# Performance work log

Measured on AMD Instinct MI355X. Metric: run time of the kernel, lower is better.

The kernel has to match this reference:

```python
import jax, jax.numpy as jnp
import numpy as np

B, S, D, H, F, L, V = 8, 512, 768, 12, 3072, 12, 30522
DK = D // H
SCALE = 1.0 / float(np.sqrt(DK))


def _ln(x, g, b, eps):
    mu = jnp.mean(x, -1, keepdims=True)
    var = jnp.mean((x - mu) ** 2, -1, keepdims=True)
    return (x - mu) / jnp.sqrt(var + eps) * g + b


def setup_inputs() -> dict:
    key = jax.random.key(0)
    ks = jax.random.split(key, 16)
    s = 0.02
    d = {
        'input_ids': jax.random.randint(ks[0], (B, S), 0, V),
        'token_type_ids': jax.random.randint(ks[1], (B, S), 0, 2),
        'attention_mask': jnp.ones((B, S), jnp.float32),
        'word_emb': jax.random.normal(ks[2], (V, D), jnp.float32) * s,
        'pos_emb': jax.random.normal(ks[3], (512, D), jnp.float32) * s,
        'type_emb': jax.random.normal(ks[4], (2, D), jnp.float32) * s,
        'emb_ln_g': jnp.ones((D,), jnp.float32),
        'emb_ln_b': jnp.zeros((D,), jnp.float32),
        # per-layer stacked params (torch Linear convention: W is [out,in])
        'Wq': jax.random.normal(ks[5], (L, D, D), jnp.float32) * s,
        'bq': jnp.zeros((L, D), jnp.float32),
        'Wk': jax.random.normal(ks[6], (L, D, D), jnp.float32) * s,
        'bk': jnp.zeros((L, D), jnp.float32),
        'Wv': jax.random.normal(ks[7], (L, D, D), jnp.float32) * s,
        'bv': jnp.zeros((L, D), jnp.float32),
        'Wo': jax.random.normal(ks[8], (L, D, D), jnp.float32) * s,
        'bo': jnp.zeros((L, D), jnp.float32),
        'attn_ln_g': jnp.ones((L, D), jnp.float32),
        'attn_ln_b': jnp.zeros((L, D), jnp.float32),
        'W1': jax.random.normal(ks[9], (L, F, D), jnp.float32) * s,
        'b1': jnp.zeros((L, F), jnp.float32),
        'W2': jax.random.normal(ks[10], (L, D, F), jnp.float32) * s,
        'b2': jnp.zeros((L, D), jnp.float32),
        'ffn_ln_g': jnp.ones((L, D), jnp.float32),
        'ffn_ln_b': jnp.zeros((L, D), jnp.float32),
    }
    return d


def reference(input_ids, token_type_ids, attention_mask, word_emb, pos_emb,
              type_emb, emb_ln_g, emb_ln_b, Wq, bq, Wk, bk, Wv, bv, Wo, bo,
              attn_ln_g, attn_ln_b, W1, b1, W2, b2, ffn_ln_g, ffn_ln_b):
    # Embeddings (dropout = identity in eval)
    x = word_emb[input_ids] + type_emb[token_type_ids] + pos_emb[:S][None]
    x = _ln(x, emb_ln_g, emb_ln_b, 1e-12)

    mask0 = attention_mask[:, None, None, :] == 0  # (B,1,1,S)

    def step(x, p):
        wq, bq_, wk, bk_, wv, bv_, wo, bo_, ag, ab, w1, b1_, w2, b2_, fg, fb = p
        q = (jnp.einsum('bsd,ed->bse', x, wq) + bq_).reshape(B, S, H, DK).transpose(0, 2, 1, 3)
        k = (jnp.einsum('bsd,ed->bse', x, wk) + bk_).reshape(B, S, H, DK).transpose(0, 2, 1, 3)
        v = (jnp.einsum('bsd,ed->bse', x, wv) + bv_).reshape(B, S, H, DK).transpose(0, 2, 1, 3)
        attn = jnp.einsum('bhqd,bhkd->bhqk', q, k) * SCALE  # (B,H,S,S)
        attn = jnp.where(mask0, -1e9, attn)
        p_attn = jax.nn.softmax(attn, axis=-1)
        ctx = jnp.einsum('bhqk,bhkd->bhqd', p_attn, v).transpose(0, 2, 1, 3).reshape(B, S, D)
        a = _ln(jnp.einsum('bsd,ed->bse', ctx, wo) + bo_ + x, ag, ab, 1e-5)
        # FFN: NO activation, and final LN has NO residual (faithful to source)
        h = jnp.einsum('bsd,fd->bsf', a, w1) + b1_
        y = jnp.einsum('bsf,df->bsd', h, w2) + b2_
        return _ln(y, fg, fb, 1e-5), None

    x, _ = jax.lax.scan(step, x, (Wq, bq, Wk, bk, Wv, bv, Wo, bo,
                                  attn_ln_g, attn_ln_b, W1, b1, W2, b2,
                                  ffn_ln_g, ffn_ln_b))
    return x
```

## Files before the change

kernel.cpp:

```cpp
#include <hip/hip_runtime.h>
#include <hip/hip_bf16.h>
#include <cstdint>
#include <cstddef>

typedef __bf16 bf16;
typedef __bf16 bf16x8 __attribute__((ext_vector_type(8)));
typedef __bf16 bf16x4 __attribute__((ext_vector_type(4)));
typedef float  floatx4 __attribute__((ext_vector_type(4)));

__device__ __forceinline__ void gload_lds16(const bf16* g, bf16* l) {
    __builtin_amdgcn_global_load_lds((const __attribute__((address_space(1))) void*)g,
                                     (__attribute__((address_space(3))) void*)l, 16, 0, 0);
}

__device__ __forceinline__ floatx4 mfma16(bf16x8 a, bf16x8 b, floatx4 c) {
    return __builtin_amdgcn_mfma_f32_16x16x32_bf16(a, b, c, 0, 0, 0);
}

template<int MODE, int TN>
__global__ __launch_bounds__(256)
void gemm_bt(const bf16* __restrict__ A, const bf16* __restrict__ Bw,
             const float* __restrict__ bias0, const float* __restrict__ bias1,
             const float* __restrict__ bias2,
             float* __restrict__ Cf, bf16* __restrict__ Cb0,
             bf16* __restrict__ Cb1, bf16* __restrict__ Cb2,
             int M, int N, int K)
{
    constexpr int NJ = TN / 32;
    __shared__ __attribute__((aligned(16))) bf16 As[128 * 32];
    __shared__ __attribute__((aligned(16))) bf16 Bs[TN * 32];

    const int tid  = threadIdx.x;
    const int lane = tid & 63;
    const int wv   = tid >> 6;
    const int quad = lane >> 4;
    const int l16  = lane & 15;
    const int m0   = blockIdx.y * 128;
    const int n0   = blockIdx.x * TN;
    const int wm   = wv & 1;
    const int wn   = wv >> 1;

    floatx4 acc[4][NJ] = {};

    const int srow = lane >> 2;
    const int scol = (lane & 3) * 8;
    const bf16* gA0 = A  + (size_t)(m0 + wv * 16 + srow) * K + scol;
    const bf16* gA1 = gA0 + (size_t)64 * K;
    const bf16* gB0 = Bw + (size_t)(n0 + wv * 16 + srow) * K + scol;
    const bf16* gB1 = gB0 + (size_t)64 * K;
    bf16* lA0 = &As[wv * 512];
    bf16* lA1 = &As[2048 + wv * 512];
    bf16* lB0 = &Bs[wv * 512];
    bf16* lB1 = &Bs[2048 + wv * 512];

    for (int k0 = 0; k0 < K; k0 += 32) {
        gload_lds16(gA0 + k0, lA0);
        gload_lds16(gA1 + k0, lA1);
        gload_lds16(gB0 + k0, lB0);
        if (TN == 128) gload_lds16(gB1 + k0, lB1);
        __syncthreads();

        bf16x8 af[4], bfr[NJ];
        #pragma unroll
        for (int i = 0; i < 4; ++i)
            af[i] = *(const bf16x8*)&As[(wm * 64 + i * 16 + l16) * 32 + quad * 8];
        #pragma unroll
        for (int j = 0; j < NJ; ++j)
            bfr[j] = *(const bf16x8*)&Bs[(wn * NJ * 16 + j * 16 + l16) * 32 + quad * 8];

        #pragma unroll
        for (int i = 0; i < 4; ++i)
            #pragma unroll
            for (int j = 0; j < NJ; ++j)
                acc[i][j] = mfma16(af[i], bfr[j], acc[i][j]);
        __syncthreads();
    }

    #pragma unroll
    for (int i = 0; i < 4; ++i) {
        const int rbase = m0 + wm * 64 + i * 16 + quad * 4;
        #pragma unroll
        for (int j = 0; j < NJ; ++j) {
            const int col = n0 + wn * NJ * 16 + j * 16 + l16;
            if (MODE == 0) {
                const float bv = bias0[col];
                #pragma unroll
                for (int r = 0; r < 4; ++r)
                    Cf[(size_t)(rbase + r) * N + col] = acc[i][j][r] + bv;
            } else if (MODE == 1) {
                const float bv = bias0[col];
                #pragma unroll
                for (int r = 0; r < 4; ++r)
                    Cb0[(size_t)(rbase + r) * N + col] = (bf16)(acc[i][j][r] + bv);
            } else {
                const int sel = col / 768;
                const int cc  = col - sel * 768;
                if (sel < 2) {
                    bf16* dst = (sel == 0) ? Cb0 : Cb1;
                    const float bv = ((sel == 0) ? bias0 : bias1)[cc];
                    #pragma unroll
                    for (int r = 0; r < 4; ++r)
                        dst[(size_t)(rbase + r) * 768 + cc] = (bf16)(acc[i][j][r] + bv);
                } else {
                    const float bv = bias2[cc];
                    const int bb = rbase >> 9, s = rbase & 511;
                    const int h = cc >> 6, d = cc & 63;
                    bf16x4 o;
                    #pragma unroll
                    for (int r = 0; r < 4; ++r) o[r] = (bf16)(acc[i][j][r] + bv);
                    *(bf16x4*)(Cb2 + (((size_t)(bb * 12 + h) * 64 + d) * 512 + s)) = o;
                }
            }
        }
    }
}

__global__ __launch_bounds__(256)
void cvt_all(const float* __restrict__ Wq, const float* __restrict__ Wk,
             const float* __restrict__ Wv, const float* __restrict__ Wo,
             const float* __restrict__ W1, const float* __restrict__ W2,
             bf16* __restrict__ out)
{
    const int l = blockIdx.y;
    const size_t i = ((size_t)blockIdx.x * 256 + threadIdx.x) * 8;
    const size_t wdd = 589824, wdf = 2359296;
    const float* src;
    size_t off;
    if      (i <  589824) { src = Wq + l * wdd; off = i; }
    else if (i < 1179648) { src = Wk + l * wdd; off = i - 589824; }
    else if (i < 1769472) { src = Wv + l * wdd; off = i - 1179648; }
    else if (i < 2359296) { src = Wo + l * wdd; off = i - 1769472; }
    else if (i < 4718592) { src = W1 + l * wdf; off = i - 2359296; }
    else                  { src = W2 + l * wdf; off = i - 4718592; }
    const float4 v0 = *(const float4*)(src + off);
    const float4 v1 = *(const float4*)(src + off + 4);
    bf16x8 o;
    o[0] = (bf16)v0.x; o[1] = (bf16)v0.y; o[2] = (bf16)v0.z; o[3] = (bf16)v0.w;
    o[4] = (bf16)v1.x; o[5] = (bf16)v1.y; o[6] = (bf16)v1.z; o[7] = (bf16)v1.w;
    *(bf16x8*)(out + (size_t)l * 7077888 + i) = o;
}

__global__ __launch_bounds__(256)
void attn3(const bf16* __restrict__ Q, const bf16* __restrict__ Kb,
           const bf16* __restrict__ VT, const float* __restrict__ mask,
           bf16* __restrict__ CTX)
{
    __shared__ __attribute__((aligned(16))) bf16 Ks[2][64 * 64];
    __shared__ __attribute__((aligned(16))) bf16 Vs[2][64 * 64];
    __shared__ __attribute__((aligned(16))) bf16 Ps[4 * 16 * 72];
    __shared__ float mb[512];

    const int tid  = threadIdx.x;
    const int lane = tid & 63;
    const int w    = tid >> 6;
    const int quad = lane >> 4;
    const int l16  = lane & 15;
    const int qt = blockIdx.x, h = blockIdx.y, b = blockIdx.z;

    mb[tid]       = (mask[b * 512 + tid] == 0.f)       ? -1e9f : -16.0f;
    mb[tid + 256] = (mask[b * 512 + tid + 256] == 0.f) ? -1e9f : -16.0f;

    bf16x8 qf0, qf1;
    {
        const bf16* qp = Q + (size_t)(b * 512 + qt * 64 + w * 16 + l16) * 768 + h * 64;
        qf0 = *(const bf16x8*)(qp + quad * 8);
        qf1 = *(const bf16x8*)(qp + 32 + quad * 8);
    }

    float lsum[4] = {0.f, 0.f, 0.f, 0.f};
    floatx4 accO[4] = {};
    bf16* pw = &Ps[w * 1152];

    const int srow8 = lane >> 3;
    const int scol8 = ((lane & 7) * 8) ^ (srow8 << 3);
    const int r0b   = w * 16;

    auto stageKV = [&](int kt, int bi) {
        #pragma unroll
        for (int i = 0; i < 2; ++i) {
            const int r0 = r0b + i * 8;
            gload_lds16(Kb + (size_t)(b * 512 + kt * 64 + r0 + srow8) * 768 + h * 64 + scol8,
                        &Ks[bi][r0 * 64]);
            gload_lds16(VT + ((size_t)(b * 12 + h) * 64 + r0 + srow8) * 512 + kt * 64 + scol8,
                        &Vs[bi][r0 * 64]);
        }
    };

    stageKV(0, 0);
    int cur = 0;
    const int swm = (l16 & 7) << 3;

    for (int kt = 0; kt < 8; ++kt) {
        __syncthreads();
        if (kt < 7) stageKV(kt + 1, cur ^ 1);

        #pragma unroll
        for (int ct = 0; ct < 4; ++ct) {
            const bf16x8 kf0 = *(const bf16x8*)&Ks[cur][(ct * 16 + l16) * 64 + ((quad * 8) ^ swm)];
            const bf16x8 kf1 = *(const bf16x8*)&Ks[cur][(ct * 16 + l16) * 64 + ((quad * 8 + 32) ^ swm)];
            floatx4 a = {0.f, 0.f, 0.f, 0.f};
            a = mfma16(qf0, kf0, a);
            a = mfma16(qf1, kf1, a);
            const float mbv = mb[kt * 64 + ct * 16 + l16];
            #pragma unroll
            for (int r = 0; r < 4; ++r) {
                const float p = __expf(fmaf(a[r], 0.125f, mbv));
                lsum[r] += p;
                pw[(quad * 4 + r) * 72 + ct * 16 + l16] = (bf16)p;
            }
        }

        #pragma unroll
        for (int kc = 0; kc < 2; ++kc) {
            const bf16x8 af = *(const bf16x8*)&pw[l16 * 72 + kc * 32 + quad * 8];
            #pragma unroll
            for (int ct2 = 0; ct2 < 4; ++ct2) {
                const bf16x8 bv = *(const bf16x8*)&Vs[cur][(ct2 * 16 + l16) * 64 + ((kc * 32 + quad * 8) ^ swm)];
                accO[ct2] = mfma16(af, bv, accO[ct2]);
            }
        }
        cur ^= 1;
    }

    float inv[4];
    #pragma unroll
    for (int r = 0; r < 4; ++r) {
        float s = lsum[r];
        #pragma unroll
        for (int o = 1; o < 16; o <<= 1) s += __shfl_xor(s, o);
        inv[r] = 1.0f / s;
    }
    #pragma unroll
    for (int ct2 = 0; ct2 < 4; ++ct2)
        #pragma unroll
        for (int r = 0; r < 4; ++r) {
            const int row = qt * 64 + w * 16 + quad * 4 + r;
            CTX[(size_t)(b * 512 + row) * 768 + h * 64 + ct2 * 16 + l16] =
                (bf16)(accO[ct2][r] * inv[r]);
        }
}

__global__ __launch_bounds__(256)
void embed_ln_k(const int* __restrict__ ids, const int* __restrict__ tts,
                const float* __restrict__ we, const float* __restrict__ pe,
                const float* __restrict__ te, const float* __restrict__ g,
                const float* __restrict__ b, float* __restrict__ X,
                bf16* __restrict__ XB)
{
    __shared__ float red[4];
    const int row = blockIdx.x;
    const int s   = row & 511;
    const int tid = threadIdx.x;
    const int id  = ids[row];
    const int tt  = tts[row];
    const float* pwp = we + (size_t)id * 768;
    const float* pt = te + (size_t)tt * 768;
    const float* pp = pe + (size_t)s * 768;
    const size_t base = (size_t)row * 768;

    float v[3];
    #pragma unroll
    for (int j = 0; j < 3; ++j) {
        const int c = tid + j * 256;
        v[j] = pwp[c] + pt[c] + pp[c];
    }
    float sm = v[0] + v[1] + v[2];
    for (int o = 32; o; o >>= 1) sm += __shfl_down(sm, o);
    if ((tid & 63) == 0) red[tid >> 6] = sm;
    __syncthreads();
    const float mu = (red[0] + red[1] + red[2] + red[3]) * (1.0f / 768.0f);
    float q = 0.f;
    #pragma unroll
    for (int j = 0; j < 3; ++j) { const float d = v[j] - mu; q += d * d; }
    __syncthreads();
    for (int o = 32; o; o >>= 1) q += __shfl_down(q, o);
    if ((tid & 63) == 0) red[tid >> 6] = q;
    __syncthreads();
    const float var  = (red[0] + red[1] + red[2] + red[3]) * (1.0f / 768.0f);
    const float rstd = rsqrtf(var + 1e-12f);
    #pragma unroll
    for (int j = 0; j < 3; ++j) {
        const int c = tid + j * 256;
        const float o = (v[j] - mu) * rstd * g[c] + b[c];
        X[base + c]  = o;
        XB[base + c] = (bf16)o;
    }
}

__global__ __launch_bounds__(256)
void ln_k(const float* T, const float* res, const float* g, const float* bta,
          float* Xo, bf16* XBo)
{
    __shared__ float red[4];
    const int row = blockIdx.x;
    const int tid = threadIdx.x;
    const size_t base = (size_t)row * 768;

    float v[3];
    #pragma unroll
    for (int j = 0; j < 3; ++j) {
        const int c = tid + j * 256;
        float x = T[base + c];
        if (res) x += res[base + c];
        v[j] = x;
    }
    float sm = v[0] + v[1] + v[2];
    for (int o = 32; o; o >>= 1) sm += __shfl_down(sm, o);
    if ((tid & 63) == 0) red[tid >> 6] = sm;
    __syncthreads();
    const float mu = (red[0] + red[1] + red[2] + red[3]) * (1.0f / 768.0f);
    float q = 0.f;
    #pragma unroll
    for (int j = 0; j < 3; ++j) { const float d = v[j] - mu; q += d * d; }
    __syncthreads();
    for (int o = 32; o; o >>= 1) q += __shfl_down(q, o);
    if ((tid & 63) == 0) red[tid >> 6] = q;
    __syncthreads();
    const float var  = (red[0] + red[1] + red[2] + red[3]) * (1.0f / 768.0f);
    const float rstd = rsqrtf(var + 1e-5f);
    #pragma unroll
    for (int j = 0; j < 3; ++j) {
        const int c = tid + j * 256;
        const float o = (v[j] - mu) * rstd * g[c] + bta[c];
        Xo[base + c]  = o;
        XBo[base + c] = (bf16)o;
    }
}

extern "C" void kernel_launch(void* const* d_in, const int* in_sizes, int n_in,
                              void* d_out, int out_size, void* d_ws, size_t ws_size,
                              hipStream_t stream)
{
    const int*   ids  = (const int*)d_in[0];
    const int*   tts  = (const int*)d_in[1];
    const float* mask = (const float*)d_in[2];
    const float* wemb = (const float*)d_in[3];
    const float* pemb = (const float*)d_in[4];
    const float* temb = (const float*)d_in[5];
    const float* eg   = (const float*)d_in[6];
    const float* eb   = (const float*)d_in[7];
    const float* Wq   = (const float*)d_in[8];
    const float* bq   = (const float*)d_in[9];
    const float* Wk   = (const float*)d_in[10];
    const float* bk   = (const float*)d_in[11];
    const float* Wv   = (const float*)d_in[12];
    const float* bv   = (const float*)d_in[13];
    const float* Wo   = (const float*)d_in[14];
    const float* bo   = (const float*)d_in[15];
    const float* ag   = (const float*)d_in[16];
    const float* ab   = (const float*)d_in[17];
    const float* W1   = (const float*)d_in[18];
    const float* b1   = (const float*)d_in[19];
    const float* W2   = (const float*)d_in[20];
    const float* b2   = (const float*)d_in[21];
    const float* fg   = (const float*)d_in[22];
    const float* fb   = (const float*)d_in[23];

    char* p = (char*)d_ws;
    float* X   = (float*)p; p += 12582912;
    bf16* XB   = (bf16*)p;  p += 6291456;
    bf16* Qb   = (bf16*)p;  p += 6291456;
    bf16* Kbuf = (bf16*)p;  p += 6291456;
    bf16* CTXb = (bf16*)p;  p += 6291456;
    float* T1  = (float*)p; p += 12582912;
    bf16* HB   = (bf16*)p;  p += 25165824;
    bf16* WB   = (bf16*)p;  p += 169869312;
    bf16* VT   = HB;

    cvt_all<<<dim3(3456, 12), 256, 0, stream>>>(Wq, Wk, Wv, Wo, W1, W2, WB);
    embed_ln_k<<<4096, 256, 0, stream>>>(ids, tts, wemb, pemb, temb, eg, eb, X, XB);

    for (int l = 0; l < 12; ++l) {
        bf16* wb = WB + (size_t)l * 7077888;
        gemm_bt<2, 128><<<dim3(18, 32), 256, 0, stream>>>(
            XB, wb, bq + l * 768, bk + l * 768, bv + l * 768,
            nullptr, Qb, Kbuf, VT, 4096, 2304, 768);
        attn3<<<dim3(8, 12, 8), 256, 0, stream>>>(Qb, Kbuf, VT, mask, CTXb);
        gemm_bt<0, 64><<<dim3(12, 32), 256, 0, stream>>>(
            CTXb, wb + 1769472, bo + l * 768, nullptr, nullptr,
            T1, nullptr, nullptr, nullptr, 4096, 768, 768);
        ln_k<<<4096, 256, 0, stream>>>(T1, X, ag + l * 768, ab + l * 768, X, XB);
        gemm_bt<1, 128><<<dim3(24, 32), 256, 0, stream>>>(
            XB, wb + 2359296, b1 + (size_t)l * 3072, nullptr, nullptr,
            nullptr, HB, nullptr, nullptr, 4096, 3072, 768);
        gemm_bt<0, 64><<<dim3(12, 32), 256, 0, stream>>>(
            HB, wb + 4718592, b2 + l * 768, nullptr, nullptr,
            T1, nullptr, nullptr, nullptr, 4096, 768, 3072);
        float* outX = (l == 11) ? (float*)d_out : X;
        ln_k<<<4096, 256, 0, stream>>>(T1, nullptr, fg + l * 768, fb + l * 768, outX, XB);
    }
}
```

Baseline: 2.621 ms.

## Double-buffer GEMM LDS, add split-K for N=768 GEMMs, remap workgroups

The GEMM now double-buffers its LDS tiles, issuing the next K-slice's global-to-LDS loads before computing the current one, which also removes one barrier per iteration. The two N=768 projections use split-K=2, writing partial sums to two fp32 buffers; the LayerNorm kernel adds them, so the grid has more workgroups on a large GPU. A workgroup index remap spreads neighbouring tiles across groups of eight, and the weight-convert kernel moves from 8-wide to 4-wide elements. In exchange there is an extra fp32 partial buffer to write and read, stored in the reused Q/K workspace, and twice the LDS per block.

```diff
diff --git a/kernel.cpp b/kernel.cpp
--- a/kernel.cpp
+++ b/kernel.cpp
@@ -17,64 +17,91 @@
     return __builtin_amdgcn_mfma_f32_16x16x32_bf16(a, b, c, 0, 0, 0);
 }
 
-template<int MODE, int TN>
+template<int MODE, int TN, int SPLITK>
 __global__ __launch_bounds__(256)
 void gemm_bt(const bf16* __restrict__ A, const bf16* __restrict__ Bw,
              const float* __restrict__ bias0, const float* __restrict__ bias1,
              const float* __restrict__ bias2,
-             float* __restrict__ Cf, bf16* __restrict__ Cb0,
-             bf16* __restrict__ Cb1, bf16* __restrict__ Cb2,
+             float* __restrict__ Cf, float* __restrict__ Cf1,
+             bf16* __restrict__ Cb0, bf16* __restrict__ Cb1,
+             bf16* __restrict__ Cb2,
              int M, int N, int K)
 {
-    constexpr int NJ = TN / 32;
-    __shared__ __attribute__((aligned(16))) bf16 As[128 * 32];
-    __shared__ __attribute__((aligned(16))) bf16 Bs[TN * 32];
+    constexpr int NJ  = TN / 32;
+    constexpr int ASZ = 128 * 32;
+    constexpr int BSZ = TN * 32;
+    __shared__ __attribute__((aligned(16))) bf16 As[2 * ASZ];
+    __shared__ __attribute__((aligned(16))) bf16 Bs[2 * BSZ];
 
     const int tid  = threadIdx.x;
     const int lane = tid & 63;
     const int wv   = tid >> 6;
     const int quad = lane >> 4;
     const int l16  = lane & 15;
-    const int m0   = blockIdx.y * 128;
-    const int n0   = blockIdx.x * TN;
-    const int wm   = wv & 1;
-    const int wn   = wv >> 1;
+
+    int bx = blockIdx.x, by = blockIdx.y;
+    {
+        const int nwg = gridDim.x * gridDim.y;
+        if ((nwg & 7) == 0) {
+            int wg = by * gridDim.x + bx;
+            wg = (wg & 7) * (nwg >> 3) + (wg >> 3);
+            bx = wg % gridDim.x;
+            by = wg / gridDim.x;
+        }
+    }
+    const int m0 = by * 128;
+    const int n0 = bx * TN;
+    const int wm = wv & 1;
+    const int wn = wv >> 1;
+
+    const int kz   = (SPLITK > 1) ? blockIdx.z : 0;
+    const int Ksub = K / SPLITK;
 
     floatx4 acc[4][NJ] = {};
 
     const int srow = lane >> 2;
     const int scol = (lane & 3) * 8;
-    const bf16* gA0 = A  + (size_t)(m0 + wv * 16 + srow) * K + scol;
+    const bf16* gA0 = A  + (size_t)(m0 + wv * 16 + srow) * K + kz * Ksub + scol;
     const bf16* gA1 = gA0 + (size_t)64 * K;
-    const bf16* gB0 = Bw + (size_t)(n0 + wv * 16 + srow) * K + scol;
+    const bf16* gB0 = Bw + (size_t)(n0 + wv * 16 + srow) * K + kz * Ksub + scol;
     const bf16* gB1 = gB0 + (size_t)64 * K;
     bf16* lA0 = &As[wv * 512];
     bf16* lA1 = &As[2048 + wv * 512];
     bf16* lB0 = &Bs[wv * 512];
     bf16* lB1 = &Bs[2048 + wv * 512];
 
-    for (int k0 = 0; k0 < K; k0 += 32) {
-        gload_lds16(gA0 + k0, lA0);
-        gload_lds16(gA1 + k0, lA1);
-        gload_lds16(gB0 + k0, lB0);
-        if (TN == 128) gload_lds16(gB1 + k0, lB1);
+    auto stage = [&](int k0, int bi) {
+        gload_lds16(gA0 + k0, lA0 + bi * ASZ);
+        gload_lds16(gA1 + k0, lA1 + bi * ASZ);
+        gload_lds16(gB0 + k0, lB0 + bi * BSZ);
+        if (TN == 128) gload_lds16(gB1 + k0, lB1 + bi * BSZ);
+    };
+
+    stage(0, 0);
+    int cur = 0;
+    for (int k0 = 0; k0 < Ksub; k0 += 32) {
         __syncthreads();
-
+        if (k0 + 32 < Ksub) stage(k0 + 32, cur ^ 1);
+
+        const bf16* Ab = &As[cur * ASZ];
+        const bf16* Bb = &Bs[cur * BSZ];
         bf16x8 af[4], bfr[NJ];
         #pragma unroll
         for (int i = 0; i < 4; ++i)
-            af[i] = *(const bf16x8*)&As[(wm * 64 + i * 16 + l16) * 32 + quad * 8];
+            af[i] = *(const bf16x8*)&Ab[(wm * 64 + i * 16 + l16) * 32 + quad * 8];
         #pragma unroll
         for (int j = 0; j < NJ; ++j)
-            bfr[j] = *(const bf16x8*)&Bs[(wn * NJ * 16 + j * 16 + l16) * 32 + quad * 8];
+            bfr[j] = *(const bf16x8*)&Bb[(wn * NJ * 16 + j * 16 + l16) * 32 + quad * 8];
 
         #pragma unroll
         for (int i = 0; i < 4; ++i)
             #pragma unroll
             for (int j = 0; j < NJ; ++j)
                 acc[i][j] = mfma16(af[i], bfr[j], acc[i][j]);
-        __syncthreads();
-    }
+        cur ^= 1;
+    }
+
+    float* dstF = (SPLITK > 1 && kz != 0) ? Cf1 : Cf;
 
     #pragma unroll
     for (int i = 0; i < 4; ++i) {
@@ -83,10 +110,10 @@
         for (int j = 0; j < NJ; ++j) {
             const int col = n0 + wn * NJ * 16 + j * 16 + l16;
             if (MODE == 0) {
-                const float bv = bias0[col];
+                const float bv = (SPLITK > 1 && kz != 0) ? 0.f : bias0[col];
                 #pragma unroll
                 for (int r = 0; r < 4; ++r)
-                    Cf[(size_t)(rbase + r) * N + col] = acc[i][j][r] + bv;
+                    dstF[(size_t)(rbase + r) * N + col] = acc[i][j][r] + bv;
             } else if (MODE == 1) {
                 const float bv = bias0[col];
                 #pragma unroll
@@ -122,7 +149,7 @@
              bf16* __restrict__ out)
 {
     const int l = blockIdx.y;
-    const size_t i = ((size_t)blockIdx.x * 256 + threadIdx.x) * 8;
+    const size_t i = ((size_t)blockIdx.x * 256 + threadIdx.x) * 4;
     const size_t wdd = 589824, wdf = 2359296;
     const float* src;
     size_t off;
@@ -132,12 +159,10 @@
     else if (i < 2359296) { src = Wo + l * wdd; off = i - 1769472; }
     else if (i < 4718592) { src = W1 + l * wdf; off = i - 2359296; }
     else                  { src = W2 + l * wdf; off = i - 4718592; }
-    const float4 v0 = *(const float4*)(src + off);
-    const float4 v1 = *(const float4*)(src + off + 4);
-    bf16x8 o;
-    o[0] = (bf16)v0.x; o[1] = (bf16)v0.y; o[2] = (bf16)v0.z; o[3] = (bf16)v0.w;
-    o[4] = (bf16)v1.x; o[5] = (bf16)v1.y; o[6] = (bf16)v1.z; o[7] = (bf16)v1.w;
-    *(bf16x8*)(out + (size_t)l * 7077888 + i) = o;
+    const float4 v = *(const float4*)(src + off);
+    bf16x4 o;
+    o[0] = (bf16)v.x; o[1] = (bf16)v.y; o[2] = (bf16)v.z; o[3] = (bf16)v.w;
+    *(bf16x4*)(out + (size_t)l * 7077888 + i) = o;
 }
 
 __global__ __launch_bounds__(256)
@@ -288,7 +313,8 @@
 }
 
 __global__ __launch_bounds__(256)
-void ln_k(const float* T, const float* res, const float* g, const float* bta,
+void ln_k(const float* T, const float* T2, const float* res,
+          const float* g, const float* bta,
           float* Xo, bf16* XBo)
 {
     __shared__ float red[4];
@@ -301,6 +327,7 @@
     for (int j = 0; j < 3; ++j) {
         const int c = tid + j * 256;
         float x = T[base + c];
+        if (T2)  x += T2[base + c];
         if (res) x += res[base + c];
         v[j] = x;
     }
@@ -366,27 +393,28 @@
     bf16* HB   = (bf16*)p;  p += 25165824;
     bf16* WB   = (bf16*)p;  p += 169869312;
     bf16* VT   = HB;
-
-    cvt_all<<<dim3(3456, 12), 256, 0, stream>>>(Wq, Wk, Wv, Wo, W1, W2, WB);
+    float* T1b = (float*)Qb;
+
+    cvt_all<<<dim3(6912, 12), 256, 0, stream>>>(Wq, Wk, Wv, Wo, W1, W2, WB);
     embed_ln_k<<<4096, 256, 0, stream>>>(ids, tts, wemb, pemb, temb, eg, eb, X, XB);
 
     for (int l = 0; l < 12; ++l) {
         bf16* wb = WB + (size_t)l * 7077888;
-        gemm_bt<2, 128><<<dim3(18, 32), 256, 0, stream>>>(
+        gemm_bt<2, 128, 1><<<dim3(18, 32), 256, 0, stream>>>(
             XB, wb, bq + l * 768, bk + l * 768, bv + l * 768,
-            nullptr, Qb, Kbuf, VT, 4096, 2304, 768);
+            nullptr, nullptr, Qb, Kbuf, VT, 4096, 2304, 768);
         attn3<<<dim3(8, 12, 8), 256, 0, stream>>>(Qb, Kbuf, VT, mask, CTXb);
-        gemm_bt<0, 64><<<dim3(12, 32), 256, 0, stream>>>(
+        gemm_bt<0, 64, 2><<<dim3(12, 32, 2), 256, 0, stream>>>(
             CTXb, wb + 1769472, bo + l * 768, nullptr, nullptr,
-            T1, nullptr, nullptr, nullptr, 4096, 768, 768);
-        ln_k<<<4096, 256, 0, stream>>>(T1, X, ag + l * 768, ab + l * 768, X, XB);
-        gemm_bt<1, 128><<<dim3(24, 32), 256, 0, stream>>>(
+            T1, T1b, nullptr, nullptr, nullptr, 4096, 768, 768);
+        ln_k<<<4096, 256, 0, stream>>>(T1, T1b, X, ag + l * 768, ab + l * 768, X, XB);
+        gemm_bt<1, 128, 1><<<dim3(24, 32), 256, 0, stream>>>(
             XB, wb + 2359296, b1 + (size_t)l * 3072, nullptr, nullptr,
-            nullptr, HB, nullptr, nullptr, 4096, 3072, 768);
-        gemm_bt<0, 64><<<dim3(12, 32), 256, 0, stream>>>(
+            nullptr, nullptr, HB, nullptr, nullptr, 4096, 3072, 768);
+        gemm_bt<0, 64, 2><<<dim3(12, 32, 2), 256, 0, stream>>>(
             HB, wb + 4718592, b2 + l * 768, nullptr, nullptr,
-            T1, nullptr, nullptr, nullptr, 4096, 768, 3072);
+            T1, T1b, nullptr, nullptr, nullptr, 4096, 768, 3072);
         float* outX = (l == 11) ? (float*)d_out : X;
-        ln_k<<<4096, 256, 0, stream>>>(T1, nullptr, fg + l * 768, fb + l * 768, outX, XB);
-    }
-}
+        ln_k<<<4096, 256, 0, stream>>>(T1, T1b, nullptr, fg + l * 768, fb + l * 768, outX, XB);
+    }
+}
```

Result: faster. 2.330 ms (-11.1%).
